# Performance work log

Measured on AMD Instinct MI355X. Metric: run time of the kernel, lower is better.

The kernel has to match this reference:

```python
import jax, jax.numpy as jnp
import numpy as np

B, T, D = 64, 512, 512
K_CODES = 256
K_FUTURE = 2


def _gru(x, w_ih, w_hh, b_ih, b_hh):
    # x: [B,T,D]; PyTorch GRU gate order: r, z, n; weights [3D, D]
    xg = jnp.einsum('btd,gd->btg', x, w_ih) + b_ih  # [B,T,3D] precomputed input gates

    def step(h, xg_t):
        hg = h @ w_hh.T + b_hh                      # [B,3D]
        xr, xz, xn = jnp.split(xg_t, 3, axis=-1)
        hr, hz, hn = jnp.split(hg, 3, axis=-1)
        r = jax.nn.sigmoid(xr + hr)
        z = jax.nn.sigmoid(xz + hz)
        n = jnp.tanh(xn + r * hn)
        h_new = (1.0 - z) * n + z * h
        return h_new, h_new

    h0 = jnp.zeros((x.shape[0], w_hh.shape[1]), x.dtype)
    _, hs = jax.lax.scan(step, h0, jnp.swapaxes(xg, 0, 1))
    return jnp.swapaxes(hs, 0, 1)  # [B,T,D]


def setup_inputs() -> dict:
    key = jax.random.key(0)
    ks = jax.random.split(key, 8)
    return {
        'features': jax.random.normal(ks[0], (B, T, D), jnp.float32),
        'codebook': jax.random.uniform(ks[1], (K_CODES, D), jnp.float32, -0.1, 0.1),
        'w_ih': jax.random.normal(ks[2], (3 * D, D), jnp.float32) * 0.02,
        'w_hh': jax.random.normal(ks[3], (3 * D, D), jnp.float32) * 0.02,
        'b_ih': jax.random.normal(ks[4], (3 * D,), jnp.float32) * 0.02,
        'b_hh': jax.random.normal(ks[5], (3 * D,), jnp.float32) * 0.02,
        'proj_w': jax.random.normal(ks[6], (D, D), jnp.float32) * 0.02,
        'proj_b': jax.random.normal(ks[7], (D,), jnp.float32) * 0.02,
    }


def reference(features, codebook, w_ih, w_hh, b_ih, b_hh, proj_w, proj_b):
    b, t, d = features.shape
    # --- quantize: cdist + argmin + gather (squared dists give same argmin) ---
    flat = features.reshape(-1, d)                              # [B*T, D]
    d2 = (jnp.sum(flat * flat, axis=1, keepdims=True)
          - 2.0 * flat @ codebook.T
          + jnp.sum(codebook * codebook, axis=1))               # [B*T, K]
    indices = jnp.argmin(d2, axis=1)                            # [B*T]
    quantized = codebook[indices].reshape(b, t, d)              # gather
    indices = indices.reshape(b, t)

    # --- context prediction loss ---
    hidden = _gru(quantized, w_ih, w_hh, b_ih, b_hh)            # [B,T,D]
    context_proj = hidden @ proj_w.T + proj_b                   # [B,T,D]
    k_max = min(K_FUTURE, t - 1)
    cp_loss = jnp.float32(0.0)
    for k in range(1, k_max + 1):
        cp_loss = cp_loss + jnp.mean((context_proj[:, :-k] - features[:, k:]) ** 2)
    cp_loss = cp_loss / k_max

    # --- VQ loss (stop_gradient mirrors torch .detach()) ---
    commitment_loss = jnp.mean((jax.lax.stop_gradient(features) - quantized) ** 2)
    codebook_loss = jnp.mean((features - jax.lax.stop_gradient(quantized)) ** 2)
    vq_loss = commitment_loss + 0.25 * codebook_loss

    total_loss = cp_loss + vq_loss
    return quantized, indices, total_loss, cp_loss, vq_loss
```

## Files before the change

kernel.cpp:

```cpp
#include <hip/hip_runtime.h>
#include <hip/hip_bf16.h>

#define B_ 64
#define T_ 512
#define D_ 512
#define K_ 256
#define G3 1536

typedef __attribute__((ext_vector_type(8))) short sh8;
typedef __attribute__((ext_vector_type(4))) short sh4;
typedef __attribute__((ext_vector_type(4))) float fx4;
typedef __attribute__((ext_vector_type(4))) int   ix4;

__device__ __forceinline__ short f2bf(float x) {
  __hip_bfloat16 h = __float2bfloat16(x);
  union { __hip_bfloat16 h; short s; } u; u.h = h; return u.s;
}
__device__ __forceinline__ float sigm(float x) { return 1.f / (1.f + __expf(-x)); }
__device__ __forceinline__ float tanh_fast(float x) {
  float e2 = __expf(-2.f * x);
  return (1.f - e2) / (1.f + e2);
}

__global__ void k_cnorm(const float* __restrict__ cb, double* __restrict__ cn) {
  int c = threadIdx.x;
  if (c < K_) {
    double s = 0.0;
    for (int k = 0; k < D_; ++k) { double v = cb[c * D_ + k]; s += v * v; }
    cn[c] = s;
  }
}

__global__ __launch_bounds__(256) void k_cg(const float* __restrict__ cb,
                                            const float* __restrict__ wih,
                                            const float* __restrict__ bih,
                                            const float* __restrict__ bhh,
                                            float* __restrict__ cg) {
  __shared__ float wl[16][512];
  int j0 = blockIdx.x * 16, c0 = blockIdx.y * 64;
  for (int v = threadIdx.x; v < 16 * 128; v += 256) {
    int r = v >> 7, q = v & 127;
    *(fx4*)&wl[r][q * 4] = *(const fx4*)&wih[(j0 + r) * D_ + q * 4];
  }
  __syncthreads();
  for (int p = threadIdx.x; p < 1024; p += 256) {
    int j = p >> 6, c = c0 + (p & 63);
    fx4 a = {0.f, 0.f, 0.f, 0.f};
    const float* cbr = &cb[c * D_];
    for (int q = 0; q < 128; ++q) {
      fx4 w4 = *(fx4*)&wl[j][q * 4];
      fx4 c4 = *(const fx4*)&cbr[q * 4];
      a += w4 * c4;
    }
    int jg = j0 + j;
    float bias = bih[jg] + (jg < 1024 ? bhh[jg] : 0.f);
    cg[c * G3 + jg] = ((a.x + a.y) + (a.z + a.w)) + bias;
  }
}

__global__ void k_cvt(const float* __restrict__ src, __hip_bfloat16* __restrict__ dst, int n4) {
  int i = blockIdx.x * blockDim.x + threadIdx.x;
  if (i < n4) {
    fx4 v = *(const fx4*)&src[i * 4];
    sh4 o; o[0] = f2bf(v.x); o[1] = f2bf(v.y); o[2] = f2bf(v.z); o[3] = f2bf(v.w);
    *(sh4*)&dst[i * 4] = o;
  }
}

__global__ __launch_bounds__(256) void k_quant(const float* __restrict__ feat,
                                               const float* __restrict__ cb,
                                               const double* __restrict__ cn,
                                               int* __restrict__ idxw,
                                               float* __restrict__ outq,
                                               float* __restrict__ outi,
                                               double* __restrict__ lacc) {
  __shared__ float fl[16][516];
  __shared__ double ss1[16][16], ss2[16][16];
  __shared__ int ii1[16][16], ii2[16][16];
  __shared__ int idxl[16];
  __shared__ float rsv[4];
  int row0 = blockIdx.x * 16;
  int tid = threadIdx.x;
  for (int v = tid; v < 16 * 128; v += 256) {
    int r = v >> 7, q = v & 127;
    *(fx4*)&fl[r][q * 4] = *(const fx4*)&feat[(row0 + r) * D_ + q * 4];
  }
  __syncthreads();
  int r = tid & 15, g = tid >> 4;
  fx4 acc[16];
#pragma unroll
  for (int c = 0; c < 16; ++c) acc[c] = (fx4){0.f, 0.f, 0.f, 0.f};
  for (int ch = 0; ch < 8; ++ch) {
    fx4 fc[16];
#pragma unroll
    for (int q = 0; q < 16; ++q) fc[q] = *(fx4*)&fl[r][ch * 64 + q * 4];
#pragma unroll
    for (int c = 0; c < 16; ++c) {
      const float* cbp = &cb[(g * 16 + c) * D_ + ch * 64];
#pragma unroll
      for (int q = 0; q < 16; ++q) {
        fx4 c4 = *(const fx4*)&cbp[q * 4];
        acc[c] += fc[q] * c4;
      }
    }
  }
  double b1 = 1e300, b2 = 1e300; int i1 = 0, i2 = 0;
#pragma unroll
  for (int c = 0; c < 16; ++c) {
    int ci = g * 16 + c;
    double dot = (double)acc[c].x + acc[c].y + acc[c].z + acc[c].w;
    double s = cn[ci] - 2.0 * dot;
    if (s < b1) { b2 = b1; i2 = i1; b1 = s; i1 = ci; }
    else if (s < b2) { b2 = s; i2 = ci; }
  }
  ss1[r][g] = b1; ss2[r][g] = b2; ii1[r][g] = i1; ii2[r][g] = i2;
  __syncthreads();
  if (tid < 16) {
    int rr = tid;
    double c1 = 1e300, c2 = 1e300; int j1 = 0, j2 = 0;
    for (int g2 = 0; g2 < 16; ++g2) {
      double s = ss1[rr][g2]; int ix = ii1[rr][g2];
      if (s < c1 || (s == c1 && ix < j1)) { c2 = c1; j2 = j1; c1 = s; j1 = ix; }
      else if (s < c2 || (s == c2 && ix < j2)) { c2 = s; j2 = ix; }
      s = ss2[rr][g2]; ix = ii2[rr][g2];
      if (s < c1 || (s == c1 && ix < j1)) { c2 = c1; j2 = j1; c1 = s; j1 = ix; }
      else if (s < c2 || (s == c2 && ix < j2)) { c2 = s; j2 = ix; }
    }
    int pick = j1;
    if (c2 - c1 < 1e-4) {
      double d1 = 0.0, d2 = 0.0;
      for (int k = 0; k < D_; ++k) {
        double fv = fl[rr][k];
        d1 += fv * (double)cb[j1 * D_ + k];
        d2 += fv * (double)cb[j2 * D_ + k];
      }
      double e1 = cn[j1] - 2.0 * d1, e2 = cn[j2] - 2.0 * d2;
      if (e2 < e1 || (e2 == e1 && j2 < j1)) pick = j2;
    }
    idxl[rr] = pick;
    idxw[row0 + rr] = pick;
    outi[row0 + rr] = (float)pick;
  }
  __syncthreads();
  float vs = 0.f;
  for (int v = tid; v < 16 * 128; v += 256) {
    int rr = v >> 7, q = v & 127;
    fx4 c4 = *(const fx4*)&cb[idxl[rr] * D_ + q * 4];
    *(fx4*)&outq[(row0 + rr) * D_ + q * 4] = c4;
    fx4 f4 = *(fx4*)&fl[rr][q * 4];
    fx4 d = f4 - c4;
    vs += d.x * d.x + d.y * d.y + d.z * d.z + d.w * d.w;
  }
#pragma unroll
  for (int off = 32; off > 0; off >>= 1) vs += __shfl_down(vs, off);
  if ((tid & 63) == 0) rsv[tid >> 6] = vs;
  __syncthreads();
  if (tid == 0) atomicAdd(&lacc[2], (double)(rsv[0] + rsv[1] + rsv[2] + rsv[3]));
}

__global__ __launch_bounds__(256, 1) void k_gru(const float* __restrict__ whh,
                                                const float* __restrict__ bhh,
                                                const float* __restrict__ cg,
                                                const int* __restrict__ idx,
                                                __hip_bfloat16* __restrict__ hid,
                                                unsigned int* __restrict__ bar,
                                                unsigned int* __restrict__ coord) {
  int tid = threadIdx.x;
  __shared__ int sh_role, sh_fast;

  if (tid == 0) {
    int xcc = 0;
    asm volatile("s_getreg_b32 %0, hwreg(HW_REG_XCC_ID)" : "=s"(xcc));
    xcc &= 7;
    unsigned slot = __hip_atomic_fetch_add(&coord[xcc], 1u, __ATOMIC_RELAXED,
                                           __HIP_MEMORY_SCOPE_AGENT);
    __hip_atomic_fetch_add(&coord[16], 1u, __ATOMIC_ACQ_REL, __HIP_MEMORY_SCOPE_AGENT);
    while (__hip_atomic_load(&coord[16], __ATOMIC_ACQUIRE, __HIP_MEMORY_SCOPE_AGENT)
           < (unsigned)gridDim.x)
      __builtin_amdgcn_s_sleep(2);

    int role = -1;
    if (slot < 8u) {
      role = xcc * 8 + (int)slot;
    } else {
      for (int x = 0; x < 8 && role < 0; ++x) {
        unsigned cx = __hip_atomic_load(&coord[x], __ATOMIC_RELAXED,
                                        __HIP_MEMORY_SCOPE_AGENT);
        unsigned have = cx < 8u ? cx : 8u;
        if (have < 8u) {
          unsigned s2 = __hip_atomic_fetch_add(&coord[8 + x], 1u, __ATOMIC_RELAXED,
                                               __HIP_MEMORY_SCOPE_AGENT);
          if (s2 < 8u - have) role = x * 8 + (int)(have + s2);
        }
      }
    }
    sh_role = role;
    int fst = 0;
    if (role >= 0) {
      unsigned cgx = __hip_atomic_load(&coord[role >> 3], __ATOMIC_RELAXED,
                                       __HIP_MEMORY_SCOPE_AGENT);
      fst = (cgx >= 8u) ? 1 : 0;
    }
    sh_fast = fst;
    __threadfence();
  }
  __syncthreads();
  const int role = sh_role;
  if (role < 0) return;
  const bool fast = (sh_fast != 0);
  const int g = role >> 3, s = role & 7;

  __builtin_amdgcn_s_setprio(1);
  int w = tid >> 6, lane = tid & 63, l15 = lane & 15, l4 = lane >> 4;

  sh8 A0[16], A1[16], A2[16];
#pragma unroll
  for (int kt = 0; kt < 16; ++kt) {
#pragma unroll
    for (int t3 = 0; t3 < 3; ++t3) {
      const float* wr = &whh[((t3 * 512) + s * 64 + w * 16 + l15) * D_];
      int k0 = kt * 32 + l4 * 8;
      fx4 x = *(const fx4*)&wr[k0];
      fx4 y = *(const fx4*)&wr[k0 + 4];
      sh8 tt;
      tt[0] = f2bf(x.x); tt[1] = f2bf(x.y); tt[2] = f2bf(x.z); tt[3] = f2bf(x.w);
      tt[4] = f2bf(y.x); tt[5] = f2bf(y.y); tt[6] = f2bf(y.z); tt[7] = f2bf(y.w);
      if (t3 == 0) A0[kt] = tt; else if (t3 == 1) A1[kt] = tt; else A2[kt] = tt;
    }
  }

  const bool act = (l15 < 8);
  const int b = l15 & 7;
  const int dg0 = s * 64 + w * 16 + l4 * 4;

  fx4 bn = *(const fx4*)&bhh[1024 + dg0];
  fx4 hp = {0.f, 0.f, 0.f, 0.f};

  unsigned* const barg = &bar[g * 32];

  int ci = act ? idx[(g * 8 + b) * T_] : 0;

  for (int t = 0; t < T_; ++t) {
    fx4 cr = {0, 0, 0, 0}, cz = {0, 0, 0, 0}, cnn = {0, 0, 0, 0};
    int ci_nx = 0;
    if (act) {
      const float* cgr = &cg[(size_t)ci * G3 + dg0];
      cr  = *(const fx4*)cgr;
      cz  = *(const fx4*)(cgr + 512);
      cnn = *(const fx4*)(cgr + 1024);
      if (t + 1 < T_) ci_nx = idx[(g * 8 + b) * T_ + t + 1];
    }

    fx4 a0 = {0, 0, 0, 0}, a1 = {0, 0, 0, 0}, a2 = {0, 0, 0, 0};
    if (t > 0) {
      const __hip_bfloat16* hrow =
          &hid[((size_t)(g * 8 + b) * T_ + (t - 1)) * D_];
#pragma unroll
      for (int kt = 0; kt < 16; ++kt) {
        sh8 bfr = {0, 0, 0, 0, 0, 0, 0, 0};
        if (act) bfr = *(const sh8*)&hrow[kt * 32 + l4 * 8];
        a0 = __builtin_amdgcn_mfma_f32_16x16x32_bf16(A0[kt], bfr, a0, 0, 0, 0);
        a1 = __builtin_amdgcn_mfma_f32_16x16x32_bf16(A1[kt], bfr, a1, 0, 0, 0);
        a2 = __builtin_amdgcn_mfma_f32_16x16x32_bf16(A2[kt], bfr, a2, 0, 0, 0);
      }
    }

    if (act) {
      sh4 hb4;
#pragma unroll
      for (int rg = 0; rg < 4; ++rg) {
        float rr = sigm(cr[rg] + a0[rg]);
        float zz = sigm(cz[rg] + a1[rg]);
        float nn = tanh_fast(cnn[rg] + rr * (a2[rg] + bn[rg]));
        float hv = (1.f - zz) * nn + zz * hp[rg];
        hp[rg] = hv;
        hb4[rg] = f2bf(hv);
      }
      *(sh4*)&hid[((size_t)(g * 8 + b) * T_ + t) * D_ + dg0] = hb4;
    }
    ci = ci_nx;

    __syncthreads();
    if (tid == 0) {
      if (!fast) __threadfence();
      __hip_atomic_fetch_add(barg, 1u, __ATOMIC_RELAXED, __HIP_MEMORY_SCOPE_AGENT);
      unsigned tgt = 8u * (unsigned)(t + 1);
      while (__hip_atomic_load(barg, __ATOMIC_RELAXED, __HIP_MEMORY_SCOPE_AGENT) < tgt)
        __builtin_amdgcn_s_sleep(1);
      if (!fast) __threadfence();
    }
    __syncthreads();
  }
}

__global__ __launch_bounds__(256) void k_proj(const __hip_bfloat16* __restrict__ hid,
                                              const __hip_bfloat16* __restrict__ pwb,
                                              const float* __restrict__ pb,
                                              const float* __restrict__ feat,
                                              double* __restrict__ lacc) {
  __shared__ char Bl[512 * 64];
  __shared__ char Al[32 * 64];
  __shared__ float rs1[4], rs2[4];
  int Mb = blockIdx.x * 32;
  int tid = threadIdx.x;
  int w = tid >> 6, lane = tid & 63, l15 = lane & 15, l4 = lane >> 4;
  fx4 acc[2][8];
#pragma unroll
  for (int a = 0; a < 2; ++a)
#pragma unroll
    for (int b = 0; b < 8; ++b) acc[a][b] = (fx4){0, 0, 0, 0};

  for (int kc = 0; kc < 16; ++kc) {
    for (int v = tid; v < 2048; v += 256) {
      int rw = v >> 2, sg = v & 3;
      ix4 d = *(const ix4*)&pwb[rw * D_ + kc * 32 + sg * 8];
      *(ix4*)(Bl + rw * 64 + ((sg * 16) ^ ((rw & 7) << 4))) = d;
    }
    if (tid < 128) {
      int rw = tid >> 2, sg = tid & 3;
      ix4 d = *(const ix4*)&hid[(size_t)(Mb + rw) * D_ + kc * 32 + sg * 8];
      *(ix4*)(Al + rw * 64 + ((sg * 16) ^ ((rw & 7) << 4))) = d;
    }
    __syncthreads();
    sh8 af0, af1;
    {
      int m = l15;
      af0 = *(const sh8*)(Al + m * 64 + ((l4 * 16) ^ ((m & 7) << 4)));
      m = 16 + l15;
      af1 = *(const sh8*)(Al + m * 64 + ((l4 * 16) ^ ((m & 7) << 4)));
    }
#pragma unroll
    for (int nt = 0; nt < 8; ++nt) {
      int n = (w * 8 + nt) * 16 + l15;
      sh8 bf = *(const sh8*)(Bl + n * 64 + ((l4 * 16) ^ ((n & 7) << 4)));
      acc[0][nt] = __builtin_amdgcn_mfma_f32_16x16x32_bf16(af0, bf, acc[0][nt], 0, 0, 0);
      acc[1][nt] = __builtin_amdgcn_mfma_f32_16x16x32_bf16(af1, bf, acc[1][nt], 0, 0, 0);
    }
    __syncthreads();
  }

  float s1 = 0.f, s2 = 0.f;
#pragma unroll
  for (int mt = 0; mt < 2; ++mt) {
#pragma unroll
    for (int nt = 0; nt < 8; ++nt) {
      int n = (w * 8 + nt) * 16 + l15;
      float bias = pb[n];
#pragma unroll
      for (int rg = 0; rg < 4; ++rg) {
        int m = Mb + mt * 16 + l4 * 4 + rg;
        float val = acc[mt][nt][rg] + bias;
        int t = m & (T_ - 1);
        if (t < T_ - 1) { float d = val - feat[(size_t)(m + 1) * D_ + n]; s1 += d * d; }
        if (t < T_ - 2) { float d = val - feat[(size_t)(m + 2) * D_ + n]; s2 += d * d; }
      }
    }
  }
#pragma unroll
  for (int off = 32; off > 0; off >>= 1) {
    s1 += __shfl_down(s1, off);
    s2 += __shfl_down(s2, off);
  }
  if (lane == 0) { rs1[w] = s1; rs2[w] = s2; }
  __syncthreads();
  if (tid == 0) {
    atomicAdd(&lacc[0], (double)rs1[0] + rs1[1] + rs1[2] + rs1[3]);
    atomicAdd(&lacc[1], (double)rs2[0] + rs2[1] + rs2[2] + rs2[3]);
  }
}

__global__ void k_fin(const double* __restrict__ lacc, float* __restrict__ outl) {
  if (threadIdx.x == 0) {
    double cp = 0.5 * (lacc[0] / ((double)B_ * (T_ - 1) * D_) +
                       lacc[1] / ((double)B_ * (T_ - 2) * D_));
    double vq = 1.25 * lacc[2] / ((double)B_ * T_ * D_);
    outl[0] = (float)(cp + vq);
    outl[1] = (float)cp;
    outl[2] = (float)vq;
  }
}

extern "C" void kernel_launch(void* const* d_in, const int* in_sizes, int n_in,
                              void* d_out, int out_size, void* d_ws, size_t ws_size,
                              hipStream_t stream) {
  (void)in_sizes; (void)n_in; (void)out_size; (void)ws_size;
  const float* feat = (const float*)d_in[0];
  const float* cb   = (const float*)d_in[1];
  const float* wih  = (const float*)d_in[2];
  const float* whh  = (const float*)d_in[3];
  const float* bih  = (const float*)d_in[4];
  const float* bhh  = (const float*)d_in[5];
  const float* pw   = (const float*)d_in[6];
  const float* pb   = (const float*)d_in[7];

  float* out  = (float*)d_out;
  float* outq = out;
  float* outi = out + (size_t)B_ * T_ * D_;
  float* outl = outi + B_ * T_;

  char* ws = (char*)d_ws;
  size_t o = 0;
  auto alloc = [&](size_t sz) { void* p = ws + o; o += (sz + 255) & ~(size_t)255; return p; };
  float*          cg    = (float*)alloc(sizeof(float) * K_ * G3);
  double*         cn    = (double*)alloc(sizeof(double) * K_);
  int*            idxw  = (int*)alloc(sizeof(int) * B_ * T_);
  __hip_bfloat16* pwb   = (__hip_bfloat16*)alloc(sizeof(__hip_bfloat16) * D_ * D_);
  double*         lacc  = (double*)alloc(sizeof(double) * 4);
  unsigned*       bar   = (unsigned*)alloc(sizeof(unsigned) * 8 * 32);
  unsigned*       coord = (unsigned*)alloc(sizeof(unsigned) * 32);
  __hip_bfloat16* hid   = (__hip_bfloat16*)alloc(sizeof(__hip_bfloat16) * (size_t)B_ * T_ * D_);

  hipMemsetAsync(lacc,  0, sizeof(double) * 4, stream);
  hipMemsetAsync(bar,   0, sizeof(unsigned) * 8 * 32, stream);
  hipMemsetAsync(coord, 0, sizeof(unsigned) * 32, stream);

  hipLaunchKernelGGL(k_cnorm, dim3(1), dim3(256), 0, stream, cb, cn);
  hipLaunchKernelGGL(k_cg, dim3(96, 4), dim3(256), 0, stream, cb, wih, bih, bhh, cg);
  hipLaunchKernelGGL(k_cvt, dim3(256), dim3(256), 0, stream, pw, pwb, D_ * D_ / 4);
  hipLaunchKernelGGL(k_quant, dim3(2048), dim3(256), 0, stream, feat, cb, cn, idxw, outq, outi, lacc);
  hipLaunchKernelGGL(k_gru, dim3(256), dim3(256), 0, stream, whh, bhh, cg, idxw, hid, bar, coord);
  hipLaunchKernelGGL(k_proj, dim3(1024), dim3(256), 0, stream, hid, pwb, pb, feat, lacc);
  hipLaunchKernelGGL(k_fin, dim3(1), dim3(64), 0, stream, lacc, outl);
}
```

Baseline: 3.290 ms.

## Fuse output projection and loss into GRU recurrence with double-buffered hidden exchange

The output projection and context-prediction loss are folded into the persistent GRU kernel: each step issues an extra MFMA on the previous hidden state against projection weights held in registers and accumulates the loss right away. The full hidden-state tensor and the separate k_proj launch go away, replaced by a small double-buffered exchange buffer per group. The gate computation is also remapped through shared memory so all 256 threads do elementwise work, the grid shrinks from 256 to 64 blocks, and barrier atomics switch to release/acquire. In exchange each step now carries more serial work (an extra MFMA, two shared-memory syncs and feature loads) on the latency-bound recurrence.

```diff
diff --git a/kernel.cpp b/kernel.cpp
--- a/kernel.cpp
+++ b/kernel.cpp
@@ -162,7 +162,11 @@
                                                 const float* __restrict__ bhh,
                                                 const float* __restrict__ cg,
                                                 const int* __restrict__ idx,
-                                                __hip_bfloat16* __restrict__ hid,
+                                                const __hip_bfloat16* __restrict__ pwb,
+                                                const float* __restrict__ pb,
+                                                const float* __restrict__ feat,
+                                                __hip_bfloat16* __restrict__ hex,
+                                                double* __restrict__ lacc,
                                                 unsigned int* __restrict__ bar,
                                                 unsigned int* __restrict__ coord) {
   int tid = threadIdx.x;
@@ -178,7 +182,6 @@
     while (__hip_atomic_load(&coord[16], __ATOMIC_ACQUIRE, __HIP_MEMORY_SCOPE_AGENT)
            < (unsigned)gridDim.x)
       __builtin_amdgcn_s_sleep(2);
-
     int role = -1;
     if (slot < 8u) {
       role = xcc * 8 + (int)slot;
@@ -210,7 +213,6 @@
   const bool fast = (sh_fast != 0);
   const int g = role >> 3, s = role & 7;
 
-  __builtin_amdgcn_s_setprio(1);
   int w = tid >> 6, lane = tid & 63, l15 = lane & 15, l4 = lane >> 4;
 
   sh8 A0[16], A1[16], A2[16];
@@ -218,7 +220,9 @@
   for (int kt = 0; kt < 16; ++kt) {
 #pragma unroll
     for (int t3 = 0; t3 < 3; ++t3) {
-      const float* wr = &whh[((t3 * 512) + s * 64 + w * 16 + l15) * D_];
+      int lr = 48 * w + 16 * t3 + l15;
+      int gate = lr >> 6, din = lr & 63;
+      const float* wr = &whh[(gate * 512 + s * 64 + din) * D_];
       int k0 = kt * 32 + l4 * 8;
       fx4 x = *(const fx4*)&wr[k0];
       fx4 y = *(const fx4*)&wr[k0 + 4];
@@ -228,144 +232,107 @@
       if (t3 == 0) A0[kt] = tt; else if (t3 == 1) A1[kt] = tt; else A2[kt] = tt;
     }
   }
+  sh8 P[16];
+#pragma unroll
+  for (int kt = 0; kt < 16; ++kt)
+    P[kt] = *(const sh8*)&pwb[(size_t)(s * 64 + w * 16 + l15) * D_ + kt * 32 + l4 * 8];
 
   const bool act = (l15 < 8);
-  const int b = l15 & 7;
-  const int dg0 = s * 64 + w * 16 + l4 * 4;
-
-  fx4 bn = *(const fx4*)&bhh[1024 + dg0];
-  fx4 hp = {0.f, 0.f, 0.f, 0.f};
+  const int bp = l15 & 7;
+  const int dgp = s * 64 + w * 16 + l4 * 4;
+  fx4 pbv = *(const fx4*)&pb[dgp];
+
+  const int d = tid & 63, b0 = tid >> 6, b1 = b0 + 4;
+  const float bn = bhh[1024 + s * 64 + d];
+
+  __shared__ float hg[192][9];
+  __shared__ float hl[8][64];
+  for (int i = tid; i < 512; i += 256) ((float*)hl)[i] = 0.f;
 
   unsigned* const barg = &bar[g * 32];
-
-  int ci = act ? idx[(g * 8 + b) * T_] : 0;
+  float s1 = 0.f, s2 = 0.f;
 
   for (int t = 0; t < T_; ++t) {
-    fx4 cr = {0, 0, 0, 0}, cz = {0, 0, 0, 0}, cnn = {0, 0, 0, 0};
-    int ci_nx = 0;
-    if (act) {
-      const float* cgr = &cg[(size_t)ci * G3 + dg0];
-      cr  = *(const fx4*)cgr;
-      cz  = *(const fx4*)(cgr + 512);
-      cnn = *(const fx4*)(cgr + 1024);
-      if (t + 1 < T_) ci_nx = idx[(g * 8 + b) * T_ + t + 1];
-    }
+    int cur = t & 1, nxt = cur ^ 1;
+    int ci0 = idx[(g * 8 + b0) * T_ + t];
+    int ci1 = idx[(g * 8 + b1) * T_ + t];
+    const float* c0p = &cg[(size_t)ci0 * G3 + s * 64 + d];
+    const float* c1p = &cg[(size_t)ci1 * G3 + s * 64 + d];
+    float cr0 = c0p[0], cz0 = c0p[512], cn0 = c0p[1024];
+    float cr1 = c1p[0], cz1 = c1p[512], cn1 = c1p[1024];
 
     fx4 a0 = {0, 0, 0, 0}, a1 = {0, 0, 0, 0}, a2 = {0, 0, 0, 0};
+    fx4 pacc = {0, 0, 0, 0};
     if (t > 0) {
-      const __hip_bfloat16* hrow =
-          &hid[((size_t)(g * 8 + b) * T_ + (t - 1)) * D_];
+      const __hip_bfloat16* hb = hex + (size_t)(cur * 8 + g) * 16 * 512;
 #pragma unroll
       for (int kt = 0; kt < 16; ++kt) {
-        sh8 bfr = {0, 0, 0, 0, 0, 0, 0, 0};
-        if (act) bfr = *(const sh8*)&hrow[kt * 32 + l4 * 8];
+        sh8 bfr = *(const sh8*)&hb[l15 * 512 + kt * 32 + l4 * 8];
         a0 = __builtin_amdgcn_mfma_f32_16x16x32_bf16(A0[kt], bfr, a0, 0, 0, 0);
         a1 = __builtin_amdgcn_mfma_f32_16x16x32_bf16(A1[kt], bfr, a1, 0, 0, 0);
         a2 = __builtin_amdgcn_mfma_f32_16x16x32_bf16(A2[kt], bfr, a2, 0, 0, 0);
-      }
-    }
-
-    if (act) {
-      sh4 hb4;
+        pacc = __builtin_amdgcn_mfma_f32_16x16x32_bf16(P[kt], bfr, pacc, 0, 0, 0);
+      }
+    }
+    if (l15 < 8) {
 #pragma unroll
       for (int rg = 0; rg < 4; ++rg) {
-        float rr = sigm(cr[rg] + a0[rg]);
-        float zz = sigm(cz[rg] + a1[rg]);
-        float nn = tanh_fast(cnn[rg] + rr * (a2[rg] + bn[rg]));
-        float hv = (1.f - zz) * nn + zz * hp[rg];
-        hp[rg] = hv;
-        hb4[rg] = f2bf(hv);
-      }
-      *(sh4*)&hid[((size_t)(g * 8 + b) * T_ + t) * D_ + dg0] = hb4;
-    }
-    ci = ci_nx;
-
+        hg[48 * w +      l4 * 4 + rg][l15] = a0[rg];
+        hg[48 * w + 16 + l4 * 4 + rg][l15] = a1[rg];
+        hg[48 * w + 32 + l4 * 4 + rg][l15] = a2[rg];
+      }
+    }
+    __syncthreads();
+    {
+      float rr = sigm(cr0 + hg[d][b0]);
+      float zz = sigm(cz0 + hg[64 + d][b0]);
+      float nn = tanh_fast(cn0 + rr * (hg[128 + d][b0] + bn));
+      float hv = (1.f - zz) * nn + zz * hl[b0][d];
+      hl[b0][d] = hv;
+      hex[(size_t)((nxt * 8 + g) * 16 + b0) * 512 + s * 64 + d] = __float2bfloat16(hv);
+      rr = sigm(cr1 + hg[d][b1]);
+      zz = sigm(cz1 + hg[64 + d][b1]);
+      nn = tanh_fast(cn1 + rr * (hg[128 + d][b1] + bn));
+      hv = (1.f - zz) * nn + zz * hl[b1][d];
+      hl[b1][d] = hv;
+      hex[(size_t)((nxt * 8 + g) * 16 + b1) * 512 + s * 64 + d] = __float2bfloat16(hv);
+    }
     __syncthreads();
     if (tid == 0) {
       if (!fast) __threadfence();
-      __hip_atomic_fetch_add(barg, 1u, __ATOMIC_RELAXED, __HIP_MEMORY_SCOPE_AGENT);
+      __hip_atomic_fetch_add(barg, 1u, __ATOMIC_RELEASE, __HIP_MEMORY_SCOPE_AGENT);
+    }
+    if (t > 0 && act) {
+      fx4 f1 = *(const fx4*)&feat[((size_t)(g * 8 + bp) * T_ + t) * D_ + dgp];
+      fx4 v = pacc + pbv;
+      fx4 d1 = v - f1;
+      s1 += d1.x * d1.x + d1.y * d1.y + d1.z * d1.z + d1.w * d1.w;
+      if (t < T_ - 1) {
+        fx4 f2 = *(const fx4*)&feat[((size_t)(g * 8 + bp) * T_ + t + 1) * D_ + dgp];
+        fx4 d2 = v - f2;
+        s2 += d2.x * d2.x + d2.y * d2.y + d2.z * d2.z + d2.w * d2.w;
+      }
+    }
+    if (tid == 0) {
       unsigned tgt = 8u * (unsigned)(t + 1);
-      while (__hip_atomic_load(barg, __ATOMIC_RELAXED, __HIP_MEMORY_SCOPE_AGENT) < tgt)
+      while (__hip_atomic_load(barg, __ATOMIC_ACQUIRE, __HIP_MEMORY_SCOPE_AGENT) < tgt)
         __builtin_amdgcn_s_sleep(1);
       if (!fast) __threadfence();
     }
     __syncthreads();
   }
-}
-
-__global__ __launch_bounds__(256) void k_proj(const __hip_bfloat16* __restrict__ hid,
-                                              const __hip_bfloat16* __restrict__ pwb,
-                                              const float* __restrict__ pb,
-                                              const float* __restrict__ feat,
-                                              double* __restrict__ lacc) {
-  __shared__ char Bl[512 * 64];
-  __shared__ char Al[32 * 64];
-  __shared__ float rs1[4], rs2[4];
-  int Mb = blockIdx.x * 32;
-  int tid = threadIdx.x;
-  int w = tid >> 6, lane = tid & 63, l15 = lane & 15, l4 = lane >> 4;
-  fx4 acc[2][8];
-#pragma unroll
-  for (int a = 0; a < 2; ++a)
-#pragma unroll
-    for (int b = 0; b < 8; ++b) acc[a][b] = (fx4){0, 0, 0, 0};
-
-  for (int kc = 0; kc < 16; ++kc) {
-    for (int v = tid; v < 2048; v += 256) {
-      int rw = v >> 2, sg = v & 3;
-      ix4 d = *(const ix4*)&pwb[rw * D_ + kc * 32 + sg * 8];
-      *(ix4*)(Bl + rw * 64 + ((sg * 16) ^ ((rw & 7) << 4))) = d;
-    }
-    if (tid < 128) {
-      int rw = tid >> 2, sg = tid & 3;
-      ix4 d = *(const ix4*)&hid[(size_t)(Mb + rw) * D_ + kc * 32 + sg * 8];
-      *(ix4*)(Al + rw * 64 + ((sg * 16) ^ ((rw & 7) << 4))) = d;
-    }
-    __syncthreads();
-    sh8 af0, af1;
-    {
-      int m = l15;
-      af0 = *(const sh8*)(Al + m * 64 + ((l4 * 16) ^ ((m & 7) << 4)));
-      m = 16 + l15;
-      af1 = *(const sh8*)(Al + m * 64 + ((l4 * 16) ^ ((m & 7) << 4)));
-    }
-#pragma unroll
-    for (int nt = 0; nt < 8; ++nt) {
-      int n = (w * 8 + nt) * 16 + l15;
-      sh8 bf = *(const sh8*)(Bl + n * 64 + ((l4 * 16) ^ ((n & 7) << 4)));
-      acc[0][nt] = __builtin_amdgcn_mfma_f32_16x16x32_bf16(af0, bf, acc[0][nt], 0, 0, 0);
-      acc[1][nt] = __builtin_amdgcn_mfma_f32_16x16x32_bf16(af1, bf, acc[1][nt], 0, 0, 0);
-    }
-    __syncthreads();
-  }
-
-  float s1 = 0.f, s2 = 0.f;
-#pragma unroll
-  for (int mt = 0; mt < 2; ++mt) {
-#pragma unroll
-    for (int nt = 0; nt < 8; ++nt) {
-      int n = (w * 8 + nt) * 16 + l15;
-      float bias = pb[n];
-#pragma unroll
-      for (int rg = 0; rg < 4; ++rg) {
-        int m = Mb + mt * 16 + l4 * 4 + rg;
-        float val = acc[mt][nt][rg] + bias;
-        int t = m & (T_ - 1);
-        if (t < T_ - 1) { float d = val - feat[(size_t)(m + 1) * D_ + n]; s1 += d * d; }
-        if (t < T_ - 2) { float d = val - feat[(size_t)(m + 2) * D_ + n]; s2 += d * d; }
-      }
-    }
-  }
+
 #pragma unroll
   for (int off = 32; off > 0; off >>= 1) {
     s1 += __shfl_down(s1, off);
     s2 += __shfl_down(s2, off);
   }
-  if (lane == 0) { rs1[w] = s1; rs2[w] = s2; }
+  __shared__ float r1[4], r2[4];
+  if (lane == 0) { r1[w] = s1; r2[w] = s2; }
   __syncthreads();
   if (tid == 0) {
-    atomicAdd(&lacc[0], (double)rs1[0] + rs1[1] + rs1[2] + rs1[3]);
-    atomicAdd(&lacc[1], (double)rs2[0] + rs2[1] + rs2[2] + rs2[3]);
+    atomicAdd(&lacc[0], (double)r1[0] + r1[1] + r1[2] + r1[3]);
+    atomicAdd(&lacc[1], (double)r2[0] + r2[1] + r2[2] + r2[3]);
   }
 }
 
@@ -408,17 +375,17 @@
   double*         lacc  = (double*)alloc(sizeof(double) * 4);
   unsigned*       bar   = (unsigned*)alloc(sizeof(unsigned) * 8 * 32);
   unsigned*       coord = (unsigned*)alloc(sizeof(unsigned) * 32);
-  __hip_bfloat16* hid   = (__hip_bfloat16*)alloc(sizeof(__hip_bfloat16) * (size_t)B_ * T_ * D_);
+  __hip_bfloat16* hex   = (__hip_bfloat16*)alloc(sizeof(__hip_bfloat16) * 2 * 8 * 16 * 512);
 
   hipMemsetAsync(lacc,  0, sizeof(double) * 4, stream);
   hipMemsetAsync(bar,   0, sizeof(unsigned) * 8 * 32, stream);
   hipMemsetAsync(coord, 0, sizeof(unsigned) * 32, stream);
+  hipMemsetAsync(hex,   0, sizeof(__hip_bfloat16) * 2 * 8 * 16 * 512, stream);
 
   hipLaunchKernelGGL(k_cnorm, dim3(1), dim3(256), 0, stream, cb, cn);
   hipLaunchKernelGGL(k_cg, dim3(96, 4), dim3(256), 0, stream, cb, wih, bih, bhh, cg);
   hipLaunchKernelGGL(k_cvt, dim3(256), dim3(256), 0, stream, pw, pwb, D_ * D_ / 4);
   hipLaunchKernelGGL(k_quant, dim3(2048), dim3(256), 0, stream, feat, cb, cn, idxw, outq, outi, lacc);
-  hipLaunchKernelGGL(k_gru, dim3(256), dim3(256), 0, stream, whh, bhh, cg, idxw, hid, bar, coord);
-  hipLaunchKernelGGL(k_proj, dim3(1024), dim3(256), 0, stream, hid, pwb, pb, feat, lacc);
+  hipLaunchKernelGGL(k_gru, dim3(64), dim3(256), 0, stream, whh, bhh, cg, idxw, pwb, pb, feat, hex, lacc, bar, coord);
   hipLaunchKernelGGL(k_fin, dim3(1), dim3(64), 0, stream, lacc, outl);
 }
```

Measured after the change: 3.440 ms. 4.6% more time.
